# Kernel optimization log

Measured on AMD Instinct MI355X. Metric: run time of the kernel, lower is better.

## Reference

```python
import jax, jax.numpy as jnp
import numpy as np

HID = 32

def _lstm_step(x, h, c, W_ih, W_hh):
    # PyTorch LSTMCell, no bias. gates: [i, f, g, o] chunks of size HID
    gates = x @ W_ih.T + h @ W_hh.T  # (B, 4*HID)
    i, f, g, o = jnp.split(gates, 4, axis=1)
    i = jax.nn.sigmoid(i)
    f = jax.nn.sigmoid(f)
    g = jnp.tanh(g)
    o = jax.nn.sigmoid(o)
    c_new = f * c + i * g
    h_new = o * jnp.tanh(c_new)
    return h_new, c_new

def setup_inputs() -> dict:
    key = jax.random.key(0)
    ks = jax.random.split(key, 5)
    T, B = 64, 65536
    poses = jax.random.normal(ks[0], (T, B, 4), dtype=jnp.float32)
    deltas = jax.random.uniform(ks[1], (T, B), dtype=jnp.float32)
    W_ih = jax.random.normal(ks[2], (4 * HID, 4), dtype=jnp.float32) * (1.0 / np.sqrt(HID))
    W_hh = jax.random.normal(ks[3], (4 * HID, HID), dtype=jnp.float32) * (1.0 / np.sqrt(HID))
    W_dense = jax.random.normal(ks[4], (3, HID), dtype=jnp.float32) * (1.0 / np.sqrt(HID))
    return {"poses": poses, "deltas": deltas, "W_ih": W_ih, "W_hh": W_hh,
            "W_dense": W_dense, "n_new_poses": T}

def reference(poses, deltas, W_ih, W_hh, W_dense, n_new_poses):
    B = poses.shape[1]
    # zip(poses, deltas) truncates encode loop to min length (source semantics)
    T_enc = min(poses.shape[0], deltas.shape[0])
    h0 = jnp.zeros((B, HID), dtype=poses.dtype)
    c0 = jnp.zeros((B, HID), dtype=poses.dtype)

    def enc_step(carry, pose):
        h, c = carry
        h, c = _lstm_step(pose, h, c, W_ih, W_hh)
        return (h, c), None

    (h, c), _ = jax.lax.scan(enc_step, (h0, c0), poses[:T_enc])

    last_velocity = h @ W_dense.T  # (B, 3)
    last_pose = poses[-1]          # (B, 4)

    def dec_step(carry, dt):
        h, c, pose, vel = carry
        cs, sn = vel[:, 1], vel[:, 2]
        norm = jnp.sqrt(cs * cs + sn * sn)
        cs = cs / norm
        sn = sn / norm
        # NOTE: source uses non-in-place .add -> positions are NOT updated; dt unused
        new_pose = jnp.concatenate([pose[:, :2], cs[:, None], sn[:, None]], axis=1)
        h, c = _lstm_step(new_pose, h, c, W_ih, W_hh)
        vel = h @ W_dense.T
        return (h, c, new_pose, vel), new_pose

    _, pred_poses = jax.lax.scan(dec_step, (h, c, last_pose, last_velocity),
                                 deltas[:n_new_poses])
    return pred_poses  # (n_new_poses, B, 4)
```

## Files before the change

### kernel.cpp

```cpp
#include <hip/hip_runtime.h>

typedef float v2f __attribute__((ext_vector_type(2)));

#define HID 32

__device__ __forceinline__ float sigmoidf_fast(float x) {
    return __fdividef(1.0f, 1.0f + __expf(-x));
}
__device__ __forceinline__ float tanhf_fast(float x) {
    return 1.0f - __fdividef(2.0f, 1.0f + __expf(2.0f * x));
}

#define PKFMA(acc, w, h) \
    asm("v_pk_fma_f32 %0, %1, %2, %0" : "+v"(acc) : "v"(w), "v"(h))

#define SWZ_ADD(p, imm) do {                                            \
    int _t = __builtin_amdgcn_ds_swizzle(__float_as_int(p), (imm));     \
    (p) += __int_as_float(_t); } while (0)
#define REDUCE32(p) do {                                                \
    SWZ_ADD(p, 0x041F); SWZ_ADD(p, 0x081F); SWZ_ADD(p, 0x101F);        \
    SWZ_ADD(p, 0x201F); SWZ_ADD(p, 0x401F); } while (0)

__global__ __launch_bounds__(256, 2)
void lstm_persist(const float* __restrict__ poses,
                  const float* __restrict__ W_ih,
                  const float* __restrict__ W_hh,
                  const float* __restrict__ W_dense,
                  float* __restrict__ out,
                  int B, int T_enc, int T_dec)
{
    __shared__ __align__(16) float hx[8][HID];

    const int tid = threadIdx.x;
    const int k   = tid & 31;
    const int eb  = tid >> 5;
    const int el  = blockIdx.x * 8 + eb;

    const v2f* Wih2 = reinterpret_cast<const v2f*>(W_ih);
    v2f wi01 = Wih2[2*k],        wi23 = Wih2[2*k + 1];
    v2f wf01 = Wih2[2*(k+32)],   wf23 = Wih2[2*(k+32) + 1];
    v2f wg01 = Wih2[2*(k+64)],   wg23 = Wih2[2*(k+64) + 1];
    v2f wo01 = Wih2[2*(k+96)],   wo23 = Wih2[2*(k+96) + 1];

    v2f whh_i[16], whh_f[16], whh_g[16], whh_o[16];
    {
        const v2f* Whh2 = reinterpret_cast<const v2f*>(W_hh);
        #pragma unroll
        for (int j = 0; j < 16; ++j) {
            whh_i[j] = Whh2[(k     ) * 16 + j];
            whh_f[j] = Whh2[(k + 32) * 16 + j];
            whh_g[j] = Whh2[(k + 64) * 16 + j];
            whh_o[j] = Whh2[(k + 96) * 16 + j];
        }
    }
    const float wd1 = W_dense[HID + k];
    const float wd2 = W_dense[2 * HID + k];

    v2f h2[16];
    #pragma unroll
    for (int j = 0; j < 16; ++j) h2[j] = (v2f){0.f, 0.f};
    float c = 0.f, hk = 0.f;

    const float4* poses4 = reinterpret_cast<const float4*>(poses);
    float4*       out4   = reinterpret_cast<float4*>(out);

    auto lstm_step = [&](float xx, float xy, float xz, float xw) {
        const v2f x01 = {xx, xy}, x23 = {xz, xw};
        v2f ai = {0.f, 0.f}, af = {0.f, 0.f}, ag = {0.f, 0.f}, ao = {0.f, 0.f};
        PKFMA(ai, wi01, x01); PKFMA(ai, wi23, x23);
        PKFMA(af, wf01, x01); PKFMA(af, wf23, x23);
        PKFMA(ag, wg01, x01); PKFMA(ag, wg23, x23);
        PKFMA(ao, wo01, x01); PKFMA(ao, wo23, x23);
        #pragma unroll
        for (int j = 0; j < 16; ++j) {
            PKFMA(ai, whh_i[j], h2[j]);
            PKFMA(af, whh_f[j], h2[j]);
            PKFMA(ag, whh_g[j], h2[j]);
            PKFMA(ao, whh_o[j], h2[j]);
        }
        const float gi = ai.x + ai.y, gf = af.x + af.y;
        const float gg = ag.x + ag.y, go = ao.x + ao.y;
        const float ii = sigmoidf_fast(gi);
        const float ff = sigmoidf_fast(gf);
        const float gt = tanhf_fast(gg);
        const float oo = sigmoidf_fast(go);
        c  = ff * c + ii * gt;
        hk = oo * tanhf_fast(c);
        hx[eb][k] = hk;
        const v2f* hr = reinterpret_cast<const v2f*>(&hx[eb][0]);
        #pragma unroll
        for (int j = 0; j < 16; ++j) h2[j] = hr[j];
    };

    float4 x = poses4[el];
    for (int t = 0; t < T_enc; ++t) {
        float4 xn = x;
        if (t + 1 < T_enc) xn = poses4[(size_t)(t + 1) * B + el];
        lstm_step(x.x, x.y, x.z, x.w);
        x = xn;
    }
    const float px = x.x, py = x.y;

    float v1 = wd1 * hk, v2 = wd2 * hk;
    REDUCE32(v1); REDUCE32(v2);

    for (int t = 0; t < T_dec; ++t) {
        const float rn = rsqrtf(v1 * v1 + v2 * v2);
        const float cs = v1 * rn, sn = v2 * rn;
        if (k == 0) out4[(size_t)t * B + el] = make_float4(px, py, cs, sn);
        lstm_step(px, py, cs, sn);
        v1 = wd1 * hk; v2 = wd2 * hk;
        REDUCE32(v1); REDUCE32(v2);
    }
}

extern "C" void kernel_launch(void* const* d_in, const int* in_sizes, int n_in,
                              void* d_out, int out_size, void* d_ws, size_t ws_size,
                              hipStream_t stream) {
    const float* poses   = (const float*)d_in[0];
    const float* W_ih    = (const float*)d_in[2];
    const float* W_hh    = (const float*)d_in[3];
    const float* W_dense = (const float*)d_in[4];
    float* out = (float*)d_out;

    const int T_enc = 64;
    const int B     = in_sizes[0] / (T_enc * 4);
    const int T_dec = out_size / (B * 4);

    dim3 grid(B / 8), block(256);
    hipLaunchKernelGGL(lstm_persist, grid, block, 0, stream,
                       poses, W_ih, W_hh, W_dense, out, B, T_enc, T_dec);
}
```

Baseline: 1.747 ms.

## Split LSTM gates across two half-waves with one batch element per wave

Each batch element now gets a full 64-lane wave instead of 32 lanes. The two half-waves each compute two of the four gates (i,g versus f,o), so each lane holds half as many W_hh registers and issues half the FMAs per step. Gate activations are exchanged with a cross-half shuffle and use exp2/rcp intrinsics directly. Occupancy hints change to allow more waves per EU. The cost is twice as many threads per element, an extra shuffle per step, and duplicated cell-state and tanh work in both halves.

```diff
diff --git a/kernel.cpp b/kernel.cpp
--- a/kernel.cpp
+++ b/kernel.cpp
@@ -3,13 +3,18 @@
 typedef float v2f __attribute__((ext_vector_type(2)));
 
 #define HID 32
+#define LOG2E 1.4426950408889634f
 
-__device__ __forceinline__ float sigmoidf_fast(float x) {
-    return __fdividef(1.0f, 1.0f + __expf(-x));
-}
-__device__ __forceinline__ float tanhf_fast(float x) {
-    return 1.0f - __fdividef(2.0f, 1.0f + __expf(2.0f * x));
-}
+#if __has_builtin(__builtin_amdgcn_exp2f)
+#define EXP2(x) __builtin_amdgcn_exp2f(x)
+#else
+#define EXP2(x) exp2f(x)
+#endif
+#if __has_builtin(__builtin_amdgcn_rcpf)
+#define RCP(x) __builtin_amdgcn_rcpf(x)
+#else
+#define RCP(x) (1.0f / (x))
+#endif
 
 #define PKFMA(acc, w, h) \
     asm("v_pk_fma_f32 %0, %1, %2, %0" : "+v"(acc) : "v"(w), "v"(h))
@@ -21,40 +26,44 @@
     SWZ_ADD(p, 0x041F); SWZ_ADD(p, 0x081F); SWZ_ADD(p, 0x101F);        \
     SWZ_ADD(p, 0x201F); SWZ_ADD(p, 0x401F); } while (0)
 
-__global__ __launch_bounds__(256, 2)
-void lstm_persist(const float* __restrict__ poses,
-                  const float* __restrict__ W_ih,
-                  const float* __restrict__ W_hh,
-                  const float* __restrict__ W_dense,
-                  float* __restrict__ out,
-                  int B, int T_enc, int T_dec)
+__global__ __attribute__((amdgpu_waves_per_eu(3, 4))) __launch_bounds__(256)
+void lstm_gatesplit(const float* __restrict__ poses,
+                    const float* __restrict__ W_ih,
+                    const float* __restrict__ W_hh,
+                    const float* __restrict__ W_dense,
+                    float* __restrict__ out,
+                    int B, int T_enc, int T_dec)
 {
-    __shared__ __align__(16) float hx[8][HID];
+    __shared__ __align__(16) float hx[4][HID];
 
-    const int tid = threadIdx.x;
-    const int k   = tid & 31;
-    const int eb  = tid >> 5;
-    const int el  = blockIdx.x * 8 + eb;
+    const int tid  = threadIdx.x;
+    const int lane = tid & 63;
+    const int wv   = tid >> 6;
+    const int k    = lane & 31;
+    const int isH  = lane >> 5;
+    const int el   = blockIdx.x * 4 + wv;
+
+    const int rowA = isH * 32 + k;
+    const int rowB = rowA + 64;
 
     const v2f* Wih2 = reinterpret_cast<const v2f*>(W_ih);
-    v2f wi01 = Wih2[2*k],        wi23 = Wih2[2*k + 1];
-    v2f wf01 = Wih2[2*(k+32)],   wf23 = Wih2[2*(k+32) + 1];
-    v2f wg01 = Wih2[2*(k+64)],   wg23 = Wih2[2*(k+64) + 1];
-    v2f wo01 = Wih2[2*(k+96)],   wo23 = Wih2[2*(k+96) + 1];
-
-    v2f whh_i[16], whh_f[16], whh_g[16], whh_o[16];
+    v2f wA0 = Wih2[2 * rowA], wA1 = Wih2[2 * rowA + 1];
+    v2f wB0 = Wih2[2 * rowB], wB1 = Wih2[2 * rowB + 1];
+    v2f whhA[16], whhB[16];
     {
         const v2f* Whh2 = reinterpret_cast<const v2f*>(W_hh);
         #pragma unroll
         for (int j = 0; j < 16; ++j) {
-            whh_i[j] = Whh2[(k     ) * 16 + j];
-            whh_f[j] = Whh2[(k + 32) * 16 + j];
-            whh_g[j] = Whh2[(k + 64) * 16 + j];
-            whh_o[j] = Whh2[(k + 96) * 16 + j];
+            whhA[j] = Whh2[rowA * 16 + j];
+            whhB[j] = Whh2[rowB * 16 + j];
         }
     }
     const float wd1 = W_dense[HID + k];
     const float wd2 = W_dense[2 * HID + k];
+
+    const float S1 = isH ? -LOG2E : 2.0f * LOG2E;
+    const float A1 = isH ? 0.0f : 1.0f;
+    const float B1 = isH ? 1.0f : -2.0f;
 
     v2f h2[16];
     #pragma unroll
@@ -64,30 +73,30 @@
     const float4* poses4 = reinterpret_cast<const float4*>(poses);
     float4*       out4   = reinterpret_cast<float4*>(out);
 
-    auto lstm_step = [&](float xx, float xy, float xz, float xw) {
-        const v2f x01 = {xx, xy}, x23 = {xz, xw};
-        v2f ai = {0.f, 0.f}, af = {0.f, 0.f}, ag = {0.f, 0.f}, ao = {0.f, 0.f};
-        PKFMA(ai, wi01, x01); PKFMA(ai, wi23, x23);
-        PKFMA(af, wf01, x01); PKFMA(af, wf23, x23);
-        PKFMA(ag, wg01, x01); PKFMA(ag, wg23, x23);
-        PKFMA(ao, wo01, x01); PKFMA(ao, wo23, x23);
+    auto lstm_step = [&](v2f x01, v2f x23) {
+        v2f aA = {0.f, 0.f}, aB = {0.f, 0.f};
+        PKFMA(aA, wA0, x01); PKFMA(aA, wA1, x23);
+        PKFMA(aB, wB0, x01); PKFMA(aB, wB1, x23);
         #pragma unroll
         for (int j = 0; j < 16; ++j) {
-            PKFMA(ai, whh_i[j], h2[j]);
-            PKFMA(af, whh_f[j], h2[j]);
-            PKFMA(ag, whh_g[j], h2[j]);
-            PKFMA(ao, whh_o[j], h2[j]);
+            PKFMA(aA, whhA[j], h2[j]);
+            PKFMA(aB, whhB[j], h2[j]);
         }
-        const float gi = ai.x + ai.y, gf = af.x + af.y;
-        const float gg = ag.x + ag.y, go = ao.x + ao.y;
-        const float ii = sigmoidf_fast(gi);
-        const float ff = sigmoidf_fast(gf);
-        const float gt = tanhf_fast(gg);
-        const float oo = sigmoidf_fast(go);
-        c  = ff * c + ii * gt;
-        hk = oo * tanhf_fast(c);
-        hx[eb][k] = hk;
-        const v2f* hr = reinterpret_cast<const v2f*>(&hx[eb][0]);
+        const float a0 = aA.x + aA.y;
+        const float a1 = aB.x + aB.y;
+        const float act0 = RCP(1.0f + EXP2(-LOG2E * a0));
+        const float act1 = fmaf(B1, RCP(1.0f + EXP2(S1 * a1)), A1);
+        const float xo0 = __shfl_xor(act0, 32, 64);
+        const float xo1 = __shfl_xor(act1, 32, 64);
+        const float i_ = isH ? xo0  : act0;
+        const float f_ = isH ? act0 : xo0;
+        const float g_ = isH ? xo1  : act1;
+        const float o_ = isH ? act1 : xo1;
+        c = fmaf(f_, c, i_ * g_);
+        const float th = fmaf(-2.0f, RCP(1.0f + EXP2((2.0f * LOG2E) * c)), 1.0f);
+        hk = o_ * th;
+        if (!isH) hx[wv][k] = hk;
+        const v2f* hr = reinterpret_cast<const v2f*>(&hx[wv][0]);
         #pragma unroll
         for (int j = 0; j < 16; ++j) h2[j] = hr[j];
     };
@@ -96,10 +105,10 @@
     for (int t = 0; t < T_enc; ++t) {
         float4 xn = x;
         if (t + 1 < T_enc) xn = poses4[(size_t)(t + 1) * B + el];
-        lstm_step(x.x, x.y, x.z, x.w);
+        lstm_step((v2f){x.x, x.y}, (v2f){x.z, x.w});
         x = xn;
     }
-    const float px = x.x, py = x.y;
+    const v2f p01 = {x.x, x.y};
 
     float v1 = wd1 * hk, v2 = wd2 * hk;
     REDUCE32(v1); REDUCE32(v2);
@@ -107,8 +116,8 @@
     for (int t = 0; t < T_dec; ++t) {
         const float rn = rsqrtf(v1 * v1 + v2 * v2);
         const float cs = v1 * rn, sn = v2 * rn;
-        if (k == 0) out4[(size_t)t * B + el] = make_float4(px, py, cs, sn);
-        lstm_step(px, py, cs, sn);
+        if (lane == 0) out4[(size_t)t * B + el] = make_float4(p01.x, p01.y, cs, sn);
+        lstm_step(p01, (v2f){cs, sn});
         v1 = wd1 * hk; v2 = wd2 * hk;
         REDUCE32(v1); REDUCE32(v2);
     }
@@ -127,7 +136,7 @@
     const int B     = in_sizes[0] / (T_enc * 4);
     const int T_dec = out_size / (B * 4);
 
-    dim3 grid(B / 8), block(256);
-    hipLaunchKernelGGL(lstm_persist, grid, block, 0, stream,
+    dim3 grid(B / 4), block(256);
+    hipLaunchKernelGGL(lstm_gatesplit, grid, block, 0, stream,
                        poses, W_ih, W_hh, W_dense, out, B, T_enc, T_dec);
 }
```

Result: faster. 1.485 ms (-15.0%).
